# Performance work log

Hardware: AMD Instinct MI355X
Metric: run time of the kernel (lower is better)

Reference implementation:

```python
import jax, jax.numpy as jnp
import numpy as np

B, H, N, M, C = 64, 8, 16384, 64, 1024
IVH = 3 * M + 6  # per-head interface size: k(M), beta, g, s(3), gamma, e(M), a(M)


def setup_inputs() -> dict:
    key = jax.random.key(0)
    k1, k2, k3, k4 = jax.random.split(key, 4)
    return {
        "x": jax.random.normal(k1, (B, C), dtype=jnp.float32),
        "current_memory": jax.random.normal(k2, (B, N, M), dtype=jnp.float32),
        "w_prev": jax.random.uniform(k3, (B, H, N), dtype=jnp.float32),
        "W": jax.random.normal(k4, (C, H * IVH), dtype=jnp.float32) * (1.0 / np.sqrt(C)),
        "b": jnp.zeros((H * IVH,), dtype=jnp.float32),
    }


def reference(x, current_memory, w_prev, W, b):
    eps = 1e-16
    iv = (x @ W + b).reshape(B, H, IVH)
    k = iv[..., :M]                                   # [B,H,M] content key
    beta = jax.nn.softplus(iv[..., M])                # [B,H] key strength
    g = jax.nn.sigmoid(iv[..., M + 1])                # [B,H] interpolation gate
    s = jax.nn.softmax(iv[..., M + 2:M + 5], axis=-1) # [B,H,3] shift weights
    gamma = 1.0 + jax.nn.softplus(iv[..., M + 5])     # [B,H] sharpening
    e = jax.nn.sigmoid(iv[..., M + 6:2 * M + 6])      # [B,H,M] erase
    a = iv[..., 2 * M + 6:3 * M + 6]                  # [B,H,M] add

    # content addressing: cosine similarity of k against every memory row
    num = jnp.einsum('bhm,bnm->bhn', k, current_memory)
    den = (jnp.linalg.norm(k, axis=-1)[..., None]
           * jnp.linalg.norm(current_memory, axis=-1)[:, None, :] + eps)
    cos = num / den                                   # [B,H,N]
    wc = jax.nn.softmax(beta[..., None] * cos, axis=-1)

    # gated interpolation with previous weighting
    wg = g[..., None] * wc + (1.0 - g[..., None]) * w_prev

    # circular conv1d shift with 3-tap kernel (shifts -1, 0, +1)
    ws = (s[..., 0:1] * jnp.roll(wg, 1, axis=-1)
          + s[..., 1:2] * wg
          + s[..., 2:3] * jnp.roll(wg, -1, axis=-1))

    # sharpening (power normalize)
    wp = ws ** gamma[..., None]
    w = wp / (jnp.sum(wp, axis=-1, keepdims=True) + eps)

    # read
    read_data = jnp.einsum('bhn,bnm->bhm', w, current_memory)
    return (read_data, w, e, a)
```

## Files before the change

kernel.cpp:

```cpp
#include <hip/hip_runtime.h>
#include <cstdint>
#include <cstddef>

#define B_    64
#define H_    8
#define N_    16384
#define M_    64
#define C_    1024
#define IVH_  198
#define J_    1584
#define CHUNK_ 256
#define NCHUNK_ 64

__device__ __forceinline__ float softplus_f(float x) {
    return (x > 20.f) ? x : log1pf(__expf(x));
}
__device__ __forceinline__ float sigmoid_f(float x) {
    return 1.f / (1.f + __expf(-x));
}

__global__ void k_gemm(const float* __restrict__ x, const float* __restrict__ W,
                       float* __restrict__ iv) {
    int lane = threadIdx.x;
    int j = blockIdx.x * 64 + lane;
    int bg = blockIdx.y;
    int c0 = blockIdx.z * 512;
    bool valid = (j < J_);
    const float* x0 = x + (size_t)(bg * 4 + 0) * C_;
    const float* x1 = x + (size_t)(bg * 4 + 1) * C_;
    const float* x2 = x + (size_t)(bg * 4 + 2) * C_;
    const float* x3 = x + (size_t)(bg * 4 + 3) * C_;
    float a0 = 0.f, a1 = 0.f, a2 = 0.f, a3 = 0.f;
    #pragma unroll 4
    for (int c = c0; c < c0 + 512; ++c) {
        float wv = valid ? W[(size_t)c * J_ + j] : 0.f;
        a0 = fmaf(x0[c], wv, a0);
        a1 = fmaf(x1[c], wv, a1);
        a2 = fmaf(x2[c], wv, a2);
        a3 = fmaf(x3[c], wv, a3);
    }
    if (valid) {
        atomicAdd(&iv[(size_t)(bg * 4 + 0) * J_ + j], a0);
        atomicAdd(&iv[(size_t)(bg * 4 + 1) * J_ + j], a1);
        atomicAdd(&iv[(size_t)(bg * 4 + 2) * J_ + j], a2);
        atomicAdd(&iv[(size_t)(bg * 4 + 3) * J_ + j], a3);
    }
}

__global__ void k_params(const float* __restrict__ iv, const float* __restrict__ bias,
                         float* __restrict__ kbuf, float* __restrict__ P,
                         float* __restrict__ out_e, float* __restrict__ out_a) {
    int bh = blockIdx.x;
    int m  = threadIdx.x;
    int b = bh >> 3, h = bh & 7;
    const float* row = iv + (size_t)b * J_ + h * IVH_;
    const float* bb  = bias + h * IVH_;
    float kv = row[m] + bb[m];
    kbuf[(size_t)bh * 64 + m] = kv;
    float s = kv * kv;
    #pragma unroll
    for (int o = 32; o > 0; o >>= 1) s += __shfl_down(s, o, 64);
    float ev = row[70 + m] + bb[70 + m];
    out_e[(size_t)bh * 64 + m] = sigmoid_f(ev);
    out_a[(size_t)bh * 64 + m] = row[134 + m] + bb[134 + m];
    if (m == 0) {
        float knorm = sqrtf(s);
        float v0 = row[64] + bb[64];
        float v1 = row[65] + bb[65];
        float v2 = row[66] + bb[66];
        float v3 = row[67] + bb[67];
        float v4 = row[68] + bb[68];
        float v5 = row[69] + bb[69];
        float beta = softplus_f(v0);
        float g = sigmoid_f(v1);
        float mx = fmaxf(v2, fmaxf(v3, v4));
        float e2 = __expf(v2 - mx), e3 = __expf(v3 - mx), e4 = __expf(v4 - mx);
        float inv = 1.f / (e2 + e3 + e4);
        float gamma = 1.f + softplus_f(v5);
        float* p = P + (size_t)bh * 8;
        p[0] = knorm; p[1] = beta; p[2] = g;
        p[3] = e2 * inv; p[4] = e3 * inv; p[5] = e4 * inv;
        p[6] = gamma;
    }
}

__global__ __launch_bounds__(256) void k_passA(
        const float* __restrict__ mem, const float* __restrict__ kbuf,
        const float* __restrict__ P, float* __restrict__ z,
        float* __restrict__ pmax, float* __restrict__ psum) {
    int b = blockIdx.y;
    int n = (blockIdx.x << 8) + threadIdx.x;
    const float4* rowp = (const float4*)(mem + ((size_t)b * N_ + n) * M_);
    float4 r[16];
    #pragma unroll
    for (int i = 0; i < 16; ++i) r[i] = rowp[i];
    float rn = 0.f;
    #pragma unroll
    for (int i = 0; i < 16; ++i)
        rn += r[i].x * r[i].x + r[i].y * r[i].y + r[i].z * r[i].z + r[i].w * r[i].w;
    rn = sqrtf(rn);
    float zv[8];
    #pragma unroll
    for (int h = 0; h < 8; ++h) {
        const float* kh = kbuf + (((size_t)b * 8 + h) << 6);
        float acc = 0.f;
        #pragma unroll
        for (int i = 0; i < 16; ++i) {
            acc = fmaf(kh[4 * i + 0], r[i].x, acc);
            acc = fmaf(kh[4 * i + 1], r[i].y, acc);
            acc = fmaf(kh[4 * i + 2], r[i].z, acc);
            acc = fmaf(kh[4 * i + 3], r[i].w, acc);
        }
        const float* p = P + (((size_t)b * 8 + h) << 3);
        float knorm = p[0], beta = p[1];
        float zz = beta * acc / (knorm * rn + 1e-16f);
        zv[h] = zz;
        z[(((size_t)b * 8 + h) << 14) + n] = zz;
    }
    __shared__ float zl[8][256];
    #pragma unroll
    for (int h = 0; h < 8; ++h) zl[h][threadIdx.x] = zv[h];
    __syncthreads();
    int w = threadIdx.x >> 6, lane = threadIdx.x & 63;
    #pragma unroll
    for (int q = 0; q < 2; ++q) {
        int h = w * 2 + q;
        float a0 = zl[h][lane], a1 = zl[h][lane + 64];
        float a2 = zl[h][lane + 128], a3 = zl[h][lane + 192];
        float mx = fmaxf(fmaxf(a0, a1), fmaxf(a2, a3));
        #pragma unroll
        for (int o = 32; o > 0; o >>= 1) mx = fmaxf(mx, __shfl_down(mx, o, 64));
        mx = __shfl(mx, 0, 64);
        float se = __expf(a0 - mx) + __expf(a1 - mx) + __expf(a2 - mx) + __expf(a3 - mx);
        #pragma unroll
        for (int o = 32; o > 0; o >>= 1) se += __shfl_down(se, o, 64);
        if (lane == 0) {
            pmax[(((size_t)b * 8 + h) << 6) + blockIdx.x] = mx;
            psum[(((size_t)b * 8 + h) << 6) + blockIdx.x] = se;
        }
    }
}

__global__ void k_stats(const float* __restrict__ pmax, const float* __restrict__ psum,
                        float* __restrict__ stats) {
    int bh = blockIdx.x * 4 + (threadIdx.x >> 6);
    int lane = threadIdx.x & 63;
    float m = pmax[((size_t)bh << 6) + lane];
    float s = psum[((size_t)bh << 6) + lane];
    float mx = m;
    #pragma unroll
    for (int o = 32; o > 0; o >>= 1) mx = fmaxf(mx, __shfl_down(mx, o, 64));
    mx = __shfl(mx, 0, 64);
    float sc = s * __expf(m - mx);
    #pragma unroll
    for (int o = 32; o > 0; o >>= 1) sc += __shfl_down(sc, o, 64);
    if (lane == 0) { stats[bh * 2] = mx; stats[bh * 2 + 1] = 1.f / sc; }
}

__global__ __launch_bounds__(256) void k_passB(
        const float* __restrict__ mem, const float* __restrict__ z,
        const float* __restrict__ wprev, const float* __restrict__ P,
        const float* __restrict__ stats, float* __restrict__ out_w,
        float* __restrict__ sumwp, float* __restrict__ readAcc) {
    __shared__ float smem[2048 + 8192];
    float* wp_s = smem;
    float* wgl  = smem + 2048;
    float* racc = smem + 2048;

    int t = threadIdx.x;
    int b = blockIdx.y;
    int n0 = blockIdx.x << 8;
    int n = n0 + t;

    #pragma unroll
    for (int h = 0; h < 8; ++h) {
        size_t bh = (size_t)b * 8 + h;
        float Mx = stats[bh * 2], iS = stats[bh * 2 + 1];
        float g = P[bh * 8 + 2];
        float wc = __expf(z[(bh << 14) + n] - Mx) * iS;
        wgl[h * 258 + t + 1] = fmaf(g, wc, (1.f - g) * wprev[(bh << 14) + n]);
    }
    if (t < 2) {
        int nh   = (t == 0) ? ((n0 + N_ - 1) & (N_ - 1)) : ((n0 + 256) & (N_ - 1));
        int slot = (t == 0) ? 0 : 257;
        #pragma unroll
        for (int h = 0; h < 8; ++h) {
            size_t bh = (size_t)b * 8 + h;
            float Mx = stats[bh * 2], iS = stats[bh * 2 + 1];
            float g = P[bh * 8 + 2];
            float wc = __expf(z[(bh << 14) + nh] - Mx) * iS;
            wgl[h * 258 + slot] = fmaf(g, wc, (1.f - g) * wprev[(bh << 14) + nh]);
        }
    }
    __syncthreads();

    float wpv[8];
    #pragma unroll
    for (int h = 0; h < 8; ++h) {
        size_t bh = (size_t)b * 8 + h;
        float s0 = P[bh * 8 + 3], s1 = P[bh * 8 + 4], s2 = P[bh * 8 + 5];
        float gam = P[bh * 8 + 6];
        float wsv = s0 * wgl[h * 258 + t] + s1 * wgl[h * 258 + t + 1]
                  + s2 * wgl[h * 258 + t + 2];
        float v = __powf(wsv, gam);
        wpv[h] = v;
        out_w[(bh << 14) + n] = v;
    }
    ((float4*)(wp_s + t * 8))[0] = make_float4(wpv[0], wpv[1], wpv[2], wpv[3]);
    ((float4*)(wp_s + t * 8))[1] = make_float4(wpv[4], wpv[5], wpv[6], wpv[7]);
    __syncthreads();

    int wv = t >> 6, lane = t & 63;
    #pragma unroll
    for (int q = 0; q < 2; ++q) {
        int h = wv * 2 + q;
        float s = wp_s[lane * 8 + h] + wp_s[(lane + 64) * 8 + h]
                + wp_s[(lane + 128) * 8 + h] + wp_s[(lane + 192) * 8 + h];
        #pragma unroll
        for (int o = 32; o > 0; o >>= 1) s += __shfl_down(s, o, 64);
        if (lane == 0) atomicAdd(&sumwp[b * 8 + h], s);
    }

    int sub = t >> 4, mq = t & 15;
    const float4* basep = (const float4*)(mem + ((size_t)b * N_ + n0) * M_);
    float4 acc[8];
    #pragma unroll
    for (int h = 0; h < 8; ++h) acc[h] = make_float4(0.f, 0.f, 0.f, 0.f);
    #pragma unroll
    for (int rr = 0; rr < 16; ++rr) {
        int row = sub * 16 + rr;
        float4 mv = basep[row * 16 + mq];
        float4 wA = ((const float4*)(wp_s + row * 8))[0];
        float4 wB = ((const float4*)(wp_s + row * 8))[1];
        float wv8[8] = {wA.x, wA.y, wA.z, wA.w, wB.x, wB.y, wB.z, wB.w};
        #pragma unroll
        for (int h = 0; h < 8; ++h) {
            acc[h].x = fmaf(wv8[h], mv.x, acc[h].x);
            acc[h].y = fmaf(wv8[h], mv.y, acc[h].y);
            acc[h].z = fmaf(wv8[h], mv.z, acc[h].z);
            acc[h].w = fmaf(wv8[h], mv.w, acc[h].w);
        }
    }
    float* rb = racc + (size_t)(sub * 16 + mq) * 32;
    #pragma unroll
    for (int h = 0; h < 8; ++h) ((float4*)rb)[h] = acc[h];
    __syncthreads();
    if (t < 128) {
        int h = t & 7, m2 = t >> 3;
        float4 s4 = make_float4(0.f, 0.f, 0.f, 0.f);
        #pragma unroll
        for (int sb = 0; sb < 16; ++sb) {
            float4 v = ((const float4*)(racc + (size_t)(sb * 16 + m2) * 32))[h];
            s4.x += v.x; s4.y += v.y; s4.z += v.z; s4.w += v.w;
        }
        float* dst = readAcc + (((size_t)b * 8 + h) << 6) + m2 * 4;
        atomicAdd(dst + 0, s4.x);
        atomicAdd(dst + 1, s4.y);
        atomicAdd(dst + 2, s4.z);
        atomicAdd(dst + 3, s4.w);
    }
}

__global__ void k_norm(float* __restrict__ out_w, const float* __restrict__ sumwp) {
    size_t idx = (size_t)blockIdx.x * 256 + threadIdx.x;
    int bh = (int)((idx * 4) >> 14);
    float inv = 1.f / (sumwp[bh] + 1e-16f);
    float4* p = (float4*)out_w + idx;
    float4 v = *p;
    v.x *= inv; v.y *= inv; v.z *= inv; v.w *= inv;
    *p = v;
}

__global__ void k_read(const float* __restrict__ readAcc, const float* __restrict__ sumwp,
                       float* __restrict__ out_rd) {
    int i = blockIdx.x * 256 + threadIdx.x;
    int bh = i >> 6;
    out_rd[i] = readAcc[i] / (sumwp[bh] + 1e-16f);
}

extern "C" void kernel_launch(void* const* d_in, const int* in_sizes, int n_in,
                              void* d_out, int out_size, void* d_ws, size_t ws_size,
                              hipStream_t stream) {
    const float* x     = (const float*)d_in[0];
    const float* mem   = (const float*)d_in[1];
    const float* wprev = (const float*)d_in[2];
    const float* W     = (const float*)d_in[3];
    const float* bias  = (const float*)d_in[4];

    float* out   = (float*)d_out;
    float* out_rd = out;
    float* out_w  = out + 32768;
    float* out_e  = out + 32768 + 8388608;
    float* out_a  = out_e + 32768;

    float* ws     = (float*)d_ws;
    float* iv      = ws;
    float* kbuf    = iv + 101376;
    float* P       = kbuf + 32768;
    float* zbuf    = P + 4096;
    float* pmax    = zbuf + 8388608;
    float* psum    = pmax + 32768;
    float* stats   = psum + 32768;
    float* sumwp   = stats + 1024;
    float* readAcc = sumwp + 512;

    hipMemsetAsync(iv, 0, (size_t)101376 * 4, stream);
    hipMemsetAsync(sumwp, 0, (size_t)(512 + 32768) * 4, stream);

    k_gemm  <<<dim3(25, 16, 2), 64, 0, stream>>>(x, W, iv);
    k_params<<<512, 64, 0, stream>>>(iv, bias, kbuf, P, out_e, out_a);
    k_passA <<<dim3(NCHUNK_, B_), 256, 0, stream>>>(mem, kbuf, P, zbuf, pmax, psum);
    k_stats <<<128, 256, 0, stream>>>(pmax, psum, stats);
    k_passB <<<dim3(NCHUNK_, B_), 256, 0, stream>>>(mem, zbuf, wprev, P, stats,
                                                    out_w, sumwp, readAcc);
    k_norm  <<<8192, 256, 0, stream>>>(out_w, sumwp);
    k_read  <<<128, 256, 0, stream>>>(readAcc, sumwp, out_rd);
}
```

Before: 655.3 us.

## Coalesce memory-row loads in passA/passB with cooperative row layout and shuffle reductions

passA no longer has each thread load one full 256-byte memory row. Groups of 16 lanes now cooperatively load rows as float4 slices and reduce the dot products and row norms with xor shuffles, giving coalesced global reads and fewer registers per thread. passB uses the same row mapping, reduces the read accumulators with shuffles into a smaller shared buffer, pads the wp_s stride, and folds the sumwp reduction into per-wave shuffles. The GEMM is retiled to 16 batches per block with a finer C split, and occupancy hints are added. In exchange it adds extra shuffle work and more atomics in the GEMM.

```diff
diff --git a/kernel.cpp b/kernel.cpp
--- a/kernel.cpp
+++ b/kernel.cpp
@@ -9,7 +9,6 @@
 #define C_    1024
 #define IVH_  198
 #define J_    1584
-#define CHUNK_ 256
 #define NCHUNK_ 64
 
 __device__ __forceinline__ float softplus_f(float x) {
@@ -19,31 +18,29 @@
     return 1.f / (1.f + __expf(-x));
 }
 
-__global__ void k_gemm(const float* __restrict__ x, const float* __restrict__ W,
-                       float* __restrict__ iv) {
+__global__ __launch_bounds__(64) void k_gemm(const float* __restrict__ x,
+                                             const float* __restrict__ W,
+                                             float* __restrict__ iv) {
     int lane = threadIdx.x;
     int j = blockIdx.x * 64 + lane;
-    int bg = blockIdx.y;
-    int c0 = blockIdx.z * 512;
     bool valid = (j < J_);
-    const float* x0 = x + (size_t)(bg * 4 + 0) * C_;
-    const float* x1 = x + (size_t)(bg * 4 + 1) * C_;
-    const float* x2 = x + (size_t)(bg * 4 + 2) * C_;
-    const float* x3 = x + (size_t)(bg * 4 + 3) * C_;
-    float a0 = 0.f, a1 = 0.f, a2 = 0.f, a3 = 0.f;
-    #pragma unroll 4
-    for (int c = c0; c < c0 + 512; ++c) {
+    int b0 = blockIdx.y * 16;
+    int c0 = blockIdx.z * 128;
+    const float* xb = x + (size_t)b0 * C_;
+    float acc[16];
+    #pragma unroll
+    for (int i = 0; i < 16; ++i) acc[i] = 0.f;
+    #pragma unroll 2
+    for (int c = c0; c < c0 + 128; ++c) {
         float wv = valid ? W[(size_t)c * J_ + j] : 0.f;
-        a0 = fmaf(x0[c], wv, a0);
-        a1 = fmaf(x1[c], wv, a1);
-        a2 = fmaf(x2[c], wv, a2);
-        a3 = fmaf(x3[c], wv, a3);
+        #pragma unroll
+        for (int bi = 0; bi < 16; ++bi)
+            acc[bi] = fmaf(xb[(size_t)bi * C_ + c], wv, acc[bi]);
     }
     if (valid) {
-        atomicAdd(&iv[(size_t)(bg * 4 + 0) * J_ + j], a0);
-        atomicAdd(&iv[(size_t)(bg * 4 + 1) * J_ + j], a1);
-        atomicAdd(&iv[(size_t)(bg * 4 + 2) * J_ + j], a2);
-        atomicAdd(&iv[(size_t)(bg * 4 + 3) * J_ + j], a3);
+        #pragma unroll
+        for (int bi = 0; bi < 16; ++bi)
+            atomicAdd(&iv[(size_t)(b0 + bi) * J_ + j], acc[bi]);
     }
 }
 
@@ -84,49 +81,58 @@
     }
 }
 
-__global__ __launch_bounds__(256) void k_passA(
+__global__ __launch_bounds__(256, 4) void k_passA(
         const float* __restrict__ mem, const float* __restrict__ kbuf,
         const float* __restrict__ P, float* __restrict__ z,
         float* __restrict__ pmax, float* __restrict__ psum) {
+    __shared__ float zl[8 * 257];
+    int t = threadIdx.x;
     int b = blockIdx.y;
-    int n = (blockIdx.x << 8) + threadIdx.x;
-    const float4* rowp = (const float4*)(mem + ((size_t)b * N_ + n) * M_);
-    float4 r[16];
-    #pragma unroll
-    for (int i = 0; i < 16; ++i) r[i] = rowp[i];
-    float rn = 0.f;
-    #pragma unroll
-    for (int i = 0; i < 16; ++i)
-        rn += r[i].x * r[i].x + r[i].y * r[i].y + r[i].z * r[i].z + r[i].w * r[i].w;
-    rn = sqrtf(rn);
-    float zv[8];
-    #pragma unroll
-    for (int h = 0; h < 8; ++h) {
-        const float* kh = kbuf + (((size_t)b * 8 + h) << 6);
-        float acc = 0.f;
-        #pragma unroll
-        for (int i = 0; i < 16; ++i) {
-            acc = fmaf(kh[4 * i + 0], r[i].x, acc);
-            acc = fmaf(kh[4 * i + 1], r[i].y, acc);
-            acc = fmaf(kh[4 * i + 2], r[i].z, acc);
-            acc = fmaf(kh[4 * i + 3], r[i].w, acc);
-        }
-        const float* p = P + (((size_t)b * 8 + h) << 3);
-        float knorm = p[0], beta = p[1];
-        float zz = beta * acc / (knorm * rn + 1e-16f);
-        zv[h] = zz;
-        z[(((size_t)b * 8 + h) << 14) + n] = zz;
-    }
-    __shared__ float zl[8][256];
-    #pragma unroll
-    for (int h = 0; h < 8; ++h) zl[h][threadIdx.x] = zv[h];
+    int n0 = blockIdx.x << 8;
+    int w = t >> 6, lane = t & 63, sub = lane >> 4, mq = lane & 15;
+
+    float4 kreg[8];
+    #pragma unroll
+    for (int h = 0; h < 8; ++h)
+        kreg[h] = *(const float4*)(kbuf + (((size_t)b * 8 + h) << 6) + mq * 4);
+    float beta = 0.f, knorm = 1.f;
+    if (mq < 8) {
+        const float* p = P + (((size_t)b * 8 + mq) << 3);
+        knorm = p[0]; beta = p[1];
+    }
+    const float* mb = mem + ((size_t)b * N_ + n0) * M_;
+
+    #pragma unroll
+    for (int rr = 0; rr < 16; ++rr) {
+        int row = (w << 6) + (rr << 2) + sub;
+        float4 mv = *(const float4*)(mb + (size_t)row * M_ + mq * 4);
+        float pr[9];
+        #pragma unroll
+        for (int h = 0; h < 8; ++h)
+            pr[h] = kreg[h].x * mv.x + kreg[h].y * mv.y
+                  + kreg[h].z * mv.z + kreg[h].w * mv.w;
+        pr[8] = mv.x * mv.x + mv.y * mv.y + mv.z * mv.z + mv.w * mv.w;
+        #pragma unroll
+        for (int o = 1; o < 16; o <<= 1) {
+            #pragma unroll
+            for (int i = 0; i < 9; ++i) pr[i] += __shfl_xor(pr[i], o, 64);
+        }
+        if (mq < 8) {
+            float rn = sqrtf(pr[8]);
+            zl[mq * 257 + row] = beta * pr[mq] / (knorm * rn + 1e-16f);
+        }
+    }
     __syncthreads();
-    int w = threadIdx.x >> 6, lane = threadIdx.x & 63;
+
+    #pragma unroll
+    for (int h = 0; h < 8; ++h)
+        z[(((size_t)b * 8 + h) << 14) + n0 + t] = zl[h * 257 + t];
+
     #pragma unroll
     for (int q = 0; q < 2; ++q) {
         int h = w * 2 + q;
-        float a0 = zl[h][lane], a1 = zl[h][lane + 64];
-        float a2 = zl[h][lane + 128], a3 = zl[h][lane + 192];
+        float a0 = zl[h * 257 + lane],       a1 = zl[h * 257 + lane + 64];
+        float a2 = zl[h * 257 + lane + 128], a3 = zl[h * 257 + lane + 192];
         float mx = fmaxf(fmaxf(a0, a1), fmaxf(a2, a3));
         #pragma unroll
         for (int o = 32; o > 0; o >>= 1) mx = fmaxf(mx, __shfl_down(mx, o, 64));
@@ -157,20 +163,22 @@
     if (lane == 0) { stats[bh * 2] = mx; stats[bh * 2 + 1] = 1.f / sc; }
 }
 
-__global__ __launch_bounds__(256) void k_passB(
+__global__ __launch_bounds__(256, 4) void k_passB(
         const float* __restrict__ mem, const float* __restrict__ z,
         const float* __restrict__ wprev, const float* __restrict__ P,
         const float* __restrict__ stats, float* __restrict__ out_w,
         float* __restrict__ sumwp, float* __restrict__ readAcc) {
-    __shared__ float smem[2048 + 8192];
-    float* wp_s = smem;
-    float* wgl  = smem + 2048;
-    float* racc = smem + 2048;
+    __shared__ float smem[3072 + 2064 + 32];
+    float* wp_s  = smem;
+    float* wgl   = smem + 3072;
+    float* racc2 = smem + 3072;
+    float* sums  = smem + 3072 + 2064;
 
     int t = threadIdx.x;
     int b = blockIdx.y;
     int n0 = blockIdx.x << 8;
     int n = n0 + t;
+    int w = t >> 6, lane = t & 63, sub = lane >> 4, mq = lane & 15;
 
     #pragma unroll
     for (int h = 0; h < 8; ++h) {
@@ -206,32 +214,29 @@
         wpv[h] = v;
         out_w[(bh << 14) + n] = v;
     }
-    ((float4*)(wp_s + t * 8))[0] = make_float4(wpv[0], wpv[1], wpv[2], wpv[3]);
-    ((float4*)(wp_s + t * 8))[1] = make_float4(wpv[4], wpv[5], wpv[6], wpv[7]);
+    #pragma unroll
+    for (int h = 0; h < 8; ++h) {
+        float s = wpv[h];
+        #pragma unroll
+        for (int o = 32; o > 0; o >>= 1) s += __shfl_down(s, o, 64);
+        if (lane == 0) sums[w * 8 + h] = s;
+    }
+    *(float4*)(wp_s + t * 12)     = make_float4(wpv[0], wpv[1], wpv[2], wpv[3]);
+    *(float4*)(wp_s + t * 12 + 4) = make_float4(wpv[4], wpv[5], wpv[6], wpv[7]);
     __syncthreads();
-
-    int wv = t >> 6, lane = t & 63;
-    #pragma unroll
-    for (int q = 0; q < 2; ++q) {
-        int h = wv * 2 + q;
-        float s = wp_s[lane * 8 + h] + wp_s[(lane + 64) * 8 + h]
-                + wp_s[(lane + 128) * 8 + h] + wp_s[(lane + 192) * 8 + h];
-        #pragma unroll
-        for (int o = 32; o > 0; o >>= 1) s += __shfl_down(s, o, 64);
-        if (lane == 0) atomicAdd(&sumwp[b * 8 + h], s);
-    }
-
-    int sub = t >> 4, mq = t & 15;
-    const float4* basep = (const float4*)(mem + ((size_t)b * N_ + n0) * M_);
+    if (t < 8)
+        atomicAdd(&sumwp[b * 8 + t], sums[t] + sums[8 + t] + sums[16 + t] + sums[24 + t]);
+
     float4 acc[8];
     #pragma unroll
     for (int h = 0; h < 8; ++h) acc[h] = make_float4(0.f, 0.f, 0.f, 0.f);
+    const float* mb = mem + ((size_t)b * N_ + n0) * M_;
     #pragma unroll
     for (int rr = 0; rr < 16; ++rr) {
-        int row = sub * 16 + rr;
-        float4 mv = basep[row * 16 + mq];
-        float4 wA = ((const float4*)(wp_s + row * 8))[0];
-        float4 wB = ((const float4*)(wp_s + row * 8))[1];
+        int row = (w << 6) + (rr << 2) + sub;
+        float4 mv = *(const float4*)(mb + (size_t)row * M_ + mq * 4);
+        float4 wA = *(const float4*)(wp_s + row * 12);
+        float4 wB = *(const float4*)(wp_s + row * 12 + 4);
         float wv8[8] = {wA.x, wA.y, wA.z, wA.w, wB.x, wB.y, wB.z, wB.w};
         #pragma unroll
         for (int h = 0; h < 8; ++h) {
@@ -241,23 +246,27 @@
             acc[h].w = fmaf(wv8[h], mv.w, acc[h].w);
         }
     }
-    float* rb = racc + (size_t)(sub * 16 + mq) * 32;
-    #pragma unroll
-    for (int h = 0; h < 8; ++h) ((float4*)rb)[h] = acc[h];
+    #pragma unroll
+    for (int h = 0; h < 8; ++h) {
+        #pragma unroll
+        for (int o = 32; o >= 16; o >>= 1) {
+            acc[h].x += __shfl_down(acc[h].x, o, 64);
+            acc[h].y += __shfl_down(acc[h].y, o, 64);
+            acc[h].z += __shfl_down(acc[h].z, o, 64);
+            acc[h].w += __shfl_down(acc[h].w, o, 64);
+        }
+    }
+    if (lane < 16) {
+        #pragma unroll
+        for (int h = 0; h < 8; ++h)
+            *(float4*)(racc2 + ((w * 8 + h) << 6) + mq * 4) = acc[h];
+    }
     __syncthreads();
-    if (t < 128) {
-        int h = t & 7, m2 = t >> 3;
-        float4 s4 = make_float4(0.f, 0.f, 0.f, 0.f);
-        #pragma unroll
-        for (int sb = 0; sb < 16; ++sb) {
-            float4 v = ((const float4*)(racc + (size_t)(sb * 16 + m2) * 32))[h];
-            s4.x += v.x; s4.y += v.y; s4.z += v.z; s4.w += v.w;
-        }
-        float* dst = readAcc + (((size_t)b * 8 + h) << 6) + m2 * 4;
-        atomicAdd(dst + 0, s4.x);
-        atomicAdd(dst + 1, s4.y);
-        atomicAdd(dst + 2, s4.z);
-        atomicAdd(dst + 3, s4.w);
+    #pragma unroll
+    for (int r = 0; r < 2; ++r) {
+        int idx = r * 256 + t;
+        float s = racc2[idx] + racc2[512 + idx] + racc2[1024 + idx] + racc2[1536 + idx];
+        atomicAdd(&readAcc[(size_t)b * 512 + idx], s);
     }
 }
 
@@ -307,7 +316,7 @@
     hipMemsetAsync(iv, 0, (size_t)101376 * 4, stream);
     hipMemsetAsync(sumwp, 0, (size_t)(512 + 32768) * 4, stream);
 
-    k_gemm  <<<dim3(25, 16, 2), 64, 0, stream>>>(x, W, iv);
+    k_gemm  <<<dim3(25, 4, 8), 64, 0, stream>>>(x, W, iv);
     k_params<<<512, 64, 0, stream>>>(iv, bias, kbuf, P, out_e, out_a);
     k_passA <<<dim3(NCHUNK_, B_), 256, 0, stream>>>(mem, kbuf, P, zbuf, pmax, psum);
     k_stats <<<128, 256, 0, stream>>>(pmax, psum, stats);
```

New measurement: 540.4 us. 1.21x faster.
